# Performance work log

Hardware: AMD Instinct MI355X
Metric: run time of the kernel (lower is better)

Reference implementation:

```python
import jax, jax.numpy as jnp
import numpy as np

NUM_FEATURES = 50


def _build_port_feature_mask(num_node_features: int = NUM_FEATURES) -> np.ndarray:
    """(F, 6) mask: port p has track if any connect/port-revenue feature for p is nonzero."""
    mask = np.zeros((num_node_features, 6), dtype=np.float32)
    feat_idx = 23
    for i in range(6):
        for j in range(i):
            mask[feat_idx, i] = 1.0
            mask[feat_idx, j] = 1.0
            feat_idx += 1
    for i in range(6):
        for k in range(2):
            mask[38 + i * 2 + k, i] = 1.0
    return mask


def setup_inputs() -> dict:
    key = jax.random.key(0)
    k1, k2 = jax.random.split(key)
    B, N, F = 16, 1024, NUM_FEATURES
    node_features = jax.random.normal(k1, (B, N, F), dtype=jnp.float32)
    direction_matrix = jax.random.randint(k2, (N, N), 0, 7, dtype=jnp.int32)
    port_feature_mask = jnp.asarray(_build_port_feature_mask(F))
    return {
        "node_features": node_features,
        "direction_matrix": direction_matrix,
        "port_feature_mask": port_feature_mask,
    }


def reference(node_features, direction_matrix, port_feature_mask):
    B, N, _ = node_features.shape
    # (B, N, 6): per-hex, per-port track indicator
    port_activity = node_features @ port_feature_mask
    port_has_track = (port_activity > 0).astype(node_features.dtype)

    dir_mat = direction_matrix.astype(jnp.int32)
    adj_mask = (dir_mat != 6).astype(node_features.dtype)  # (N, N)
    dir_clamped = jnp.minimum(dir_mat, 5)                  # (N, N)
    opp_clamped = jnp.minimum((dir_mat + 3) % 6, 5)        # (N, N)

    i_idx = jnp.arange(N)[:, None]  # row index i, broadcasts with (N, N)
    j_idx = jnp.arange(N)[None, :]  # col index j
    # src[b, i, j] = port_has_track[b, i, dir_clamped[i, j]]
    src_ports = port_has_track[:, i_idx, dir_clamped]  # (B, N, N)
    # dst[b, i, j] = port_has_track[b, j, opp_clamped[i, j]]
    dst_ports = port_has_track[:, j_idx, opp_clamped]  # (B, N, N)

    return src_ports * dst_ports * adj_mask[None, :, :]
```

## Files before the change

### kernel.cpp

```cpp
#include <hip/hip_runtime.h>

#define N_NODES 1024
#define B_SZ 16
#define F_SZ 50

typedef float f32x4 __attribute__((ext_vector_type(4)));

__global__ __launch_bounds__(64) void ports_kernel(
        const float* __restrict__ nf,
        unsigned char* __restrict__ bitsT) {
    int idx = blockIdx.x * 64 + threadIdx.x;
    int b = idx >> 10;
    int n = idx & (N_NODES - 1);
    const float* r = nf + (size_t)idx * F_SZ;

    float f[27];
    #pragma unroll
    for (int q = 0; q < 27; ++q) f[q] = r[23 + q];

    float a0 = (((((f[0]  + f[1])  + f[3])  + f[6])  + f[10]) + f[15]) + f[16];
    float a1 = (((((f[0]  + f[2])  + f[4])  + f[7])  + f[11]) + f[17]) + f[18];
    float a2 = (((((f[1]  + f[2])  + f[5])  + f[8])  + f[12]) + f[19]) + f[20];
    float a3 = (((((f[3]  + f[4])  + f[5])  + f[9])  + f[13]) + f[21]) + f[22];
    float a4 = (((((f[6]  + f[7])  + f[8])  + f[9])  + f[14]) + f[23]) + f[24];
    float a5 = (((((f[10] + f[11]) + f[12]) + f[13]) + f[14]) + f[25]) + f[26];

    unsigned m = 0;
    m |= (a0 > 0.0f) ? 1u  : 0u;
    m |= (a1 > 0.0f) ? 2u  : 0u;
    m |= (a2 > 0.0f) ? 4u  : 0u;
    m |= (a3 > 0.0f) ? 8u  : 0u;
    m |= (a4 > 0.0f) ? 16u : 0u;
    m |= (a5 > 0.0f) ? 32u : 0u;
    bitsT[n * B_SZ + b] = (unsigned char)m;
}

__global__ __launch_bounds__(256) void connect_kernel(
        const int* __restrict__ dir,
        const unsigned char* __restrict__ bitsT,
        float* __restrict__ out) {
    const int i = blockIdx.x;
    const int t = threadIdx.x;

    int4 d = ((const int4*)(dir + (size_t)i * N_NODES))[t];
    int dv[4] = {d.x, d.y, d.z, d.w};
    unsigned ds[4], os[4], am[4];
    #pragma unroll
    for (int k = 0; k < 4; ++k) {
        am[k] = (dv[k] != 6) ? 1u : 0u;
        ds[k] = (unsigned)min(dv[k], 5);
        os[k] = (unsigned)min((dv[k] + 3) % 6, 5);
    }

    const uint4* bt = (const uint4*)bitsT;
    uint4 srcv = bt[i];
    unsigned srcw[4] = {srcv.x, srcv.y, srcv.z, srcv.w};
    unsigned dstw[4][4];
    #pragma unroll
    for (int k = 0; k < 4; ++k) {
        uint4 v = bt[t * 4 + k];
        dstw[k][0] = v.x; dstw[k][1] = v.y; dstw[k][2] = v.z; dstw[k][3] = v.w;
    }

    float* obase = out + (size_t)i * N_NODES + (size_t)t * 4;
    const int rot = i & 15;
    #pragma unroll
    for (int bb = 0; bb < B_SZ; ++bb) {
        const int b = (bb + rot) & 15;
        unsigned s = (srcw[b >> 2] >> ((b & 3) * 8)) & 0x3fu;
        f32x4 o;
        #pragma unroll
        for (int k = 0; k < 4; ++k) {
            unsigned tb = (dstw[k][b >> 2] >> ((b & 3) * 8)) & 0x3fu;
            o[k] = ((s >> ds[k]) & (tb >> os[k]) & am[k] & 1u) ? 1.0f : 0.0f;
        }
        __builtin_nontemporal_store(
            o, (f32x4*)(obase + (size_t)b * N_NODES * N_NODES));
    }
}

extern "C" void kernel_launch(void* const* d_in, const int* in_sizes, int n_in,
                              void* d_out, int out_size, void* d_ws, size_t ws_size,
                              hipStream_t stream) {
    const float* nf   = (const float*)d_in[0];
    const int*   dir  = (const int*)d_in[1];
    float* out = (float*)d_out;
    unsigned char* bitsT = (unsigned char*)d_ws;

    ports_kernel<<<(B_SZ * N_NODES) / 64, 64, 0, stream>>>(nf, bitsT);
    connect_kernel<<<N_NODES, 256, 0, stream>>>(dir, bitsT, out);
}
```

Before: 23.82 us.

## Tile connect kernel over contiguous output rows instead of batch-strided rows

The port-bit layout changes from node-major transposed to batch-major. The connect kernel now gives each block 4 consecutive output rows (b,i) instead of one row i across all 16 batches. Blocks now write contiguous output memory rather than 16 regions a full batch apart, and there are 16x more, smaller blocks. In exchange the direction matrix is reloaded once per batch instead of once for all batches, which relies on L2 reuse.

```diff
diff --git a/kernel.cpp b/kernel.cpp
--- a/kernel.cpp
+++ b/kernel.cpp
@@ -8,10 +8,8 @@
 
 __global__ __launch_bounds__(64) void ports_kernel(
         const float* __restrict__ nf,
-        unsigned char* __restrict__ bitsT) {
+        unsigned char* __restrict__ bits) {
     int idx = blockIdx.x * 64 + threadIdx.x;
-    int b = idx >> 10;
-    int n = idx & (N_NODES - 1);
     const float* r = nf + (size_t)idx * F_SZ;
 
     float f[27];
@@ -32,61 +30,52 @@
     m |= (a3 > 0.0f) ? 8u  : 0u;
     m |= (a4 > 0.0f) ? 16u : 0u;
     m |= (a5 > 0.0f) ? 32u : 0u;
-    bitsT[n * B_SZ + b] = (unsigned char)m;
+    bits[idx] = (unsigned char)m;
 }
 
 __global__ __launch_bounds__(256) void connect_kernel(
         const int* __restrict__ dir,
-        const unsigned char* __restrict__ bitsT,
+        const unsigned char* __restrict__ bits,
         float* __restrict__ out) {
-    const int i = blockIdx.x;
+    const int q = blockIdx.x;
     const int t = threadIdx.x;
+    const int p0 = q * 4;
+    const int b = p0 >> 10;
 
-    int4 d = ((const int4*)(dir + (size_t)i * N_NODES))[t];
-    int dv[4] = {d.x, d.y, d.z, d.w};
-    unsigned ds[4], os[4], am[4];
+    uchar4 dv4 = ((const uchar4*)(bits + b * N_NODES))[t];
+    unsigned tb[4] = {dv4.x, dv4.y, dv4.z, dv4.w};
+
     #pragma unroll
-    for (int k = 0; k < 4; ++k) {
-        am[k] = (dv[k] != 6) ? 1u : 0u;
-        ds[k] = (unsigned)min(dv[k], 5);
-        os[k] = (unsigned)min((dv[k] + 3) % 6, 5);
-    }
+    for (int r = 0; r < 4; ++r) {
+        const int p = p0 + r;
+        const int i = p & (N_NODES - 1);
 
-    const uint4* bt = (const uint4*)bitsT;
-    uint4 srcv = bt[i];
-    unsigned srcw[4] = {srcv.x, srcv.y, srcv.z, srcv.w};
-    unsigned dstw[4][4];
-    #pragma unroll
-    for (int k = 0; k < 4; ++k) {
-        uint4 v = bt[t * 4 + k];
-        dstw[k][0] = v.x; dstw[k][1] = v.y; dstw[k][2] = v.z; dstw[k][3] = v.w;
-    }
+        int4 d = ((const int4*)(dir + (size_t)i * N_NODES))[t];
+        int dvv[4] = {d.x, d.y, d.z, d.w};
+        unsigned s = bits[b * N_NODES + i];
 
-    float* obase = out + (size_t)i * N_NODES + (size_t)t * 4;
-    const int rot = i & 15;
-    #pragma unroll
-    for (int bb = 0; bb < B_SZ; ++bb) {
-        const int b = (bb + rot) & 15;
-        unsigned s = (srcw[b >> 2] >> ((b & 3) * 8)) & 0x3fu;
         f32x4 o;
         #pragma unroll
         for (int k = 0; k < 4; ++k) {
-            unsigned tb = (dstw[k][b >> 2] >> ((b & 3) * 8)) & 0x3fu;
-            o[k] = ((s >> ds[k]) & (tb >> os[k]) & am[k] & 1u) ? 1.0f : 0.0f;
+            int dval = dvv[k];
+            unsigned am = (dval != 6) ? 1u : 0u;
+            unsigned ds = (unsigned)min(dval, 5);
+            unsigned os = (unsigned)min((dval + 3) % 6, 5);
+            o[k] = ((s >> ds) & (tb[k] >> os) & am & 1u) ? 1.0f : 0.0f;
         }
         __builtin_nontemporal_store(
-            o, (f32x4*)(obase + (size_t)b * N_NODES * N_NODES));
+            o, (f32x4*)(out + (size_t)p * N_NODES) + t);
     }
 }
 
 extern "C" void kernel_launch(void* const* d_in, const int* in_sizes, int n_in,
                               void* d_out, int out_size, void* d_ws, size_t ws_size,
                               hipStream_t stream) {
-    const float* nf   = (const float*)d_in[0];
-    const int*   dir  = (const int*)d_in[1];
+    const float* nf  = (const float*)d_in[0];
+    const int*   dir = (const int*)d_in[1];
     float* out = (float*)d_out;
-    unsigned char* bitsT = (unsigned char*)d_ws;
+    unsigned char* bits = (unsigned char*)d_ws;
 
-    ports_kernel<<<(B_SZ * N_NODES) / 64, 64, 0, stream>>>(nf, bitsT);
-    connect_kernel<<<N_NODES, 256, 0, stream>>>(dir, bitsT, out);
+    ports_kernel<<<(B_SZ * N_NODES) / 64, 64, 0, stream>>>(nf, bits);
+    connect_kernel<<<(B_SZ * N_NODES) / 4, 256, 0, stream>>>(dir, bits, out);
 }
```

Result: faster. 21.10 us (-11.4%).
